# Kernel tuning notes

Measured on AMD Instinct MI355X. Metric: run time of the kernel, lower is better.

Reference implementation:

```python
import jax, jax.numpy as jnp
import numpy as np

N, E, B = 50000, 800000, 128
IN, HID, OUT, H = 256, 256, 256, 4
NEG_SLOPE = 0.2
EPS_BN = 1e-5
EPS_LN = 1e-5


def setup_inputs() -> dict:
    key = jax.random.key(0)
    ks = jax.random.split(key, 10)
    C1, C2 = HID // H, OUT // H
    s = lambda k, sh: jax.random.normal(k, sh, jnp.float32) * 0.05
    return dict(
        x=jax.random.normal(ks[0], (N, IN), jnp.float32),
        edge_index=jax.random.randint(ks[1], (2, E), 0, N),
        batch=jnp.sort(jax.random.randint(ks[2], (N,), 0, B)),
        W1=s(ks[3], (IN, HID)), a_src1=s(ks[4], (H, C1)), a_dst1=s(ks[5], (H, C1)),
        b1=jnp.zeros((HID,), jnp.float32),
        bn1_g=jnp.ones((HID,), jnp.float32), bn1_b=jnp.zeros((HID,), jnp.float32),
        bn1_m=jnp.zeros((HID,), jnp.float32), bn1_v=jnp.ones((HID,), jnp.float32),
        ln1_g=jnp.ones((HID,), jnp.float32), ln1_b=jnp.zeros((HID,), jnp.float32),
        W2=s(ks[6], (HID + IN, OUT)), a_src2=s(ks[7], (H, C2)), a_dst2=s(ks[8], (H, C2)),
        b2=jnp.zeros((OUT,), jnp.float32),
        bn2_g=jnp.ones((OUT,), jnp.float32), bn2_b=jnp.zeros((OUT,), jnp.float32),
        bn2_m=jnp.zeros((OUT,), jnp.float32), bn2_v=jnp.ones((OUT,), jnp.float32),
        ln2_g=jnp.ones((OUT,), jnp.float32), ln2_b=jnp.zeros((OUT,), jnp.float32),
    )


def gat_conv(x, edge_index, W, a_s, a_d, b):
    # PyG GATConv (concat heads, add_self_loops=True, eval -> no attention dropout)
    n = x.shape[0]
    Hh, C = a_s.shape
    h = (x @ W).reshape(n, Hh, C)                      # [N,H,C]
    loop = jnp.arange(n)
    src = jnp.concatenate([edge_index[0], loop])       # [E+N]
    dst = jnp.concatenate([edge_index[1], loop])
    al_s = jnp.einsum('nhc,hc->nh', h, a_s)            # [N,H]
    al_d = jnp.einsum('nhc,hc->nh', h, a_d)
    e = jax.nn.leaky_relu(al_s[src] + al_d[dst], NEG_SLOPE)   # [E+N,H]
    emax = jax.ops.segment_max(e, dst, num_segments=n)        # segment softmax over incoming edges
    p = jnp.exp(e - emax[dst])
    denom = jax.ops.segment_sum(p, dst, num_segments=n)
    alpha = p / (denom[dst] + 1e-16)
    out = jax.ops.segment_sum(alpha[:, :, None] * h[src], dst, num_segments=n)
    return out.reshape(n, Hh * C) + b


def bn_eval(x, g, b, m, v):
    return (x - m) * (g * jax.lax.rsqrt(v + EPS_BN)) + b


def layer_norm(x, g, b):
    mu = jnp.mean(x, axis=-1, keepdims=True)
    var = jnp.mean(jnp.square(x - mu), axis=-1, keepdims=True)
    return (x - mu) * jax.lax.rsqrt(var + EPS_LN) * g + b


def reference(x, edge_index, batch,
              W1, a_src1, a_dst1, b1, bn1_g, bn1_b, bn1_m, bn1_v, ln1_g, ln1_b,
              W2, a_src2, a_dst2, b2, bn2_g, bn2_b, bn2_m, bn2_v, ln2_g, ln2_b):
    x1 = x
    h = gat_conv(x, edge_index, W1, a_src1, a_dst1, b1)
    h = jax.nn.relu(layer_norm(bn_eval(h, bn1_g, bn1_b, bn1_m, bn1_v), ln1_g, ln1_b))
    x2 = h
    # root_extend: broadcast the first node of each (sorted) batch segment
    root_idx = jnp.searchsorted(batch, jnp.arange(B))  # first occurrence per graph
    h = jnp.concatenate([h, x1[root_idx[batch]]], axis=1)
    h = gat_conv(h, edge_index, W2, a_src2, a_dst2, b2)
    h = jax.nn.relu(layer_norm(bn_eval(h, bn2_g, bn2_b, bn2_m, bn2_v), ln2_g, ln2_b))
    h = jnp.concatenate([h, x2[root_idx[batch]]], axis=1)   # [N, OUT+HID]
    sums = jax.ops.segment_sum(h, batch, num_segments=B)
    cnt = jax.ops.segment_sum(jnp.ones((h.shape[0],), h.dtype), batch, num_segments=B)
    return sums / jnp.maximum(cnt, 1.0)[:, None]            # scatter_mean -> [B, OUT+HID]
```

## Files before the change

### kernel.cpp

```cpp
#include <hip/hip_runtime.h>
#include <stdint.h>

typedef unsigned short u16;
typedef unsigned int u32;
typedef unsigned char u8;
typedef __bf16 bf16x8 __attribute__((ext_vector_type(8)));
typedef float f32x4 __attribute__((ext_vector_type(4)));

#define NGRAPH 128

__device__ __forceinline__ float b2f(u16 u) {
    union { u32 i; float f; } c; c.i = ((u32)u) << 16; return c.f;
}
__device__ __forceinline__ u16 f2b(float f) {
    union { float f; u32 i; } c; c.f = f;
    u32 r = c.i + 0x7fffu + ((c.i >> 16) & 1u);
    return (u16)(r >> 16);
}
__device__ __forceinline__ float s8x(u32 v, int k) {
    return (float)((int)(v << (24 - 8 * k)) >> 24);
}

__global__ void k_sentinel(u16* __restrict__ out, int n, u16 pat) {
    int i = blockIdx.x * 256 + threadIdx.x;
    if (i < n) out[i] = pat;
}

__global__ __launch_bounds__(256) void k_init(const u16* __restrict__ x, const int* __restrict__ batch,
                                              int* __restrict__ deg, float* __restrict__ pool,
                                              int* __restrict__ flag, int* __restrict__ root,
                                              int N, int B) {
    __shared__ int cnt;
    int i = blockIdx.x * 256 + threadIdx.x;
    if (i < N + 1) deg[i] = 0;
    if (i < B * 256) pool[i] = 0.0f;
    if (blockIdx.x == 0) {
        if (threadIdx.x == 0) cnt = 0;
        __syncthreads();
        int weird = 0;
        for (int k = threadIdx.x; k < 4096; k += 256) {
            u16 u = x[2 * k];
            int e = (u >> 7) & 0xff;
            if (e != 0 && (e < 100 || e > 140)) weird++;
        }
        atomicAdd(&cnt, weird);
        __syncthreads();
        if (threadIdx.x == 0) *flag = (cnt > 1024) ? 1 : 0;
    } else if (blockIdx.x == 1) {
        int b = threadIdx.x;
        if (b <= B) {
            int lo = 0, hi = N;
            while (lo < hi) { int mid = (lo + hi) >> 1; if (batch[mid] < b) lo = mid + 1; else hi = mid; }
            root[b] = lo;
        }
    }
}

__global__ __launch_bounds__(256) void k_cvt4(const void* __restrict__ src, u16* __restrict__ dst,
                                              int n4, const int* __restrict__ flag) {
    int i = blockIdx.x * 256 + threadIdx.x;
    if (i >= n4) return;
    if (*flag) {
        float4 v = ((const float4*)src)[i];
        ushort4 o;
        o.x = f2b(v.x); o.y = f2b(v.y); o.z = f2b(v.z); o.w = f2b(v.w);
        ((ushort4*)dst)[i] = o;
    } else {
        ((ushort4*)dst)[i] = ((const ushort4*)src)[i];
    }
}

__global__ __launch_bounds__(256) void k_cvt_small(
    const void* p0, const void* p1, const void* p2, const void* p3, const void* p4,
    const void* p5, const void* p6, const void* p7, const void* p8, const void* p9,
    const void* p10, const void* p11, const void* p12, const void* p13, const void* p14,
    const void* p15, const void* p16, const void* p17,
    u16* __restrict__ dst, const int* __restrict__ flag) {
    const void* ps[18] = {p0,p1,p2,p3,p4,p5,p6,p7,p8,p9,p10,p11,p12,p13,p14,p15,p16,p17};
    int f = *flag;
    int vec = blockIdx.x;
    int j = threadIdx.x;
    const void* s = ps[vec];
    dst[vec * 256 + j] = f ? f2b(((const float*)s)[j]) : ((const u16*)s)[j];
}

__global__ __launch_bounds__(256) void k_tr2(const u16* __restrict__ w1, u16* __restrict__ wt1,
                                             const u16* __restrict__ w2, u16* __restrict__ wt2) {
    int idx = blockIdx.x * 256 + threadIdx.x;
    int halfsel = idx >> 16;
    int j = idx & 65535;
    int n = j >> 8, k = j & 255;
    if (halfsel == 0) wt1[n * 256 + k] = w1[k * 256 + n];
    else              wt2[n * 256 + k] = w2[k * 256 + n];
}

__global__ __launch_bounds__(256) void k_hist(const int* __restrict__ ei, int* __restrict__ deg, int E) {
    int e = blockIdx.x * 256 + threadIdx.x;
    if (e < E) atomicAdd(&deg[ei[E + e]], 1);
}

__global__ __launch_bounds__(256) void k_scan1(const int* __restrict__ in, int* __restrict__ out,
                                               int* __restrict__ bsums, int total) {
    __shared__ int lds[256];
    int tid = threadIdx.x;
    int base = blockIdx.x * 2048 + tid * 8;
    int v[8]; int ts = 0;
#pragma unroll
    for (int r = 0; r < 8; r++) { int i = base + r; int x = (i < total) ? in[i] : 0; v[r] = x; ts += x; }
    lds[tid] = ts;
    __syncthreads();
    for (int off = 1; off < 256; off <<= 1) {
        int t = (tid >= off) ? lds[tid - off] : 0;
        __syncthreads();
        lds[tid] += t;
        __syncthreads();
    }
    int run = lds[tid] - ts;
#pragma unroll
    for (int r = 0; r < 8; r++) { int i = base + r; if (i < total) out[i] = run; run += v[r]; }
    if (tid == 255) bsums[blockIdx.x] = lds[255];
}

__global__ void k_scan2(int* __restrict__ bsums, int nb) {
    if (threadIdx.x == 0 && blockIdx.x == 0) {
        int run = 0;
        for (int i = 0; i < nb; i++) { int t = bsums[i]; bsums[i] = run; run += t; }
    }
}

__global__ __launch_bounds__(256) void k_scan3(const int* __restrict__ pscan, const int* __restrict__ bsums,
                                               int* __restrict__ ptr, int* __restrict__ cursor,
                                               int total, int N) {
    int i = blockIdx.x * 256 + threadIdx.x;
    if (i >= total) return;
    int val = pscan[i] + bsums[i >> 11];
    ptr[i] = val;
    if (i < N) cursor[i] = val;
}

__global__ __launch_bounds__(256) void k_fill(const int* __restrict__ ei, int* __restrict__ cursor,
                                              int* __restrict__ csr, int E) {
    int e = blockIdx.x * 256 + threadIdx.x;
    if (e < E) {
        int src = ei[e];
        int pos = atomicAdd(&cursor[ei[E + e]], 1);
        csr[pos] = src;
    }
}

__global__ __launch_bounds__(256) void k_gemm(const u16* __restrict__ A, const u16* __restrict__ Bt,
                                              u16* __restrict__ C, u8* __restrict__ C8,
                                              float* __restrict__ salsc, int M,
                                              const float* __restrict__ r2, const int* __restrict__ batch) {
    __shared__ __align__(16) u16 smem[128 * 64 * 2];
    u16* As = smem;
    u16* Bs = smem + 128 * 64;
    const int tid = threadIdx.x;
    const int lane = tid & 63;
    const int wave = tid >> 6;
    const int bm = blockIdx.x >> 1;
    const int bn = blockIdx.x & 1;
    const int m0 = bm * 128, n0 = bn * 128;
    const int wm = wave >> 1, wn = wave & 1;
    const int lm = lane & 15, lq = lane >> 4;
    f32x4 acc[4][4] = {};

    for (int k0 = 0; k0 < 256; k0 += 64) {
        uint4 ra[4], rb[4];
#pragma unroll
        for (int it = 0; it < 4; ++it) {
            int t = tid + 256 * it;
            int m = t >> 3;
            int kc = (t & 7) ^ (m & 7);
            int gm = m0 + m; if (gm > M - 1) gm = M - 1;
            ra[it] = *(const uint4*)(A + (size_t)gm * 256 + k0 + kc * 8);
            rb[it] = *(const uint4*)(Bt + (size_t)(n0 + m) * 256 + k0 + kc * 8);
        }
        __syncthreads();
#pragma unroll
        for (int it = 0; it < 4; ++it) {
            int t = tid + 256 * it;
            *(uint4*)(As + t * 8) = ra[it];
            *(uint4*)(Bs + t * 8) = rb[it];
        }
        __syncthreads();
#pragma unroll
        for (int ks = 0; ks < 2; ++ks) {
            int kq = ks * 4 + lq;
            bf16x8 af[4], bfr[4];
#pragma unroll
            for (int i = 0; i < 4; i++) {
                int m = wm * 64 + i * 16 + lm;
                af[i] = *(const bf16x8*)(As + (m * 8 + (kq ^ (m & 7))) * 8);
                int n = wn * 64 + i * 16 + lm;
                bfr[i] = *(const bf16x8*)(Bs + (n * 8 + (kq ^ (n & 7))) * 8);
            }
#pragma unroll
            for (int i = 0; i < 4; i++)
#pragma unroll
                for (int j = 0; j < 4; j++)
                    acc[i][j] = __builtin_amdgcn_mfma_f32_16x16x32_bf16(af[i], bfr[j], acc[i][j], 0, 0, 0);
        }
    }

    __syncthreads();
    u8* lds8 = (u8*)smem;
#pragma unroll
    for (int i = 0; i < 4; i++) {
#pragma unroll
        for (int r = 0; r < 4; r++) {
            int rl = wm * 64 + i * 16 + lq * 4 + r;
            int row = m0 + rl;
            bool ok = (row < M);
            const float* r2row = (r2 && ok) ? (r2 + (size_t)batch[row] * 256) : nullptr;
            float v[4];
#pragma unroll
            for (int j = 0; j < 4; j++) {
                v[j] = acc[i][j][r];
                if (r2row) v[j] += r2row[n0 + wn * 64 + j * 16 + lm];
            }
            float mx = fmaxf(fmaxf(fabsf(v[0]), fabsf(v[1])), fmaxf(fabsf(v[2]), fabsf(v[3])));
#pragma unroll
            for (int off = 1; off < 16; off <<= 1) mx = fmaxf(mx, __shfl_xor(mx, off));
            float scl = mx * (1.0f / 127.0f);
            float isc = (mx > 0.f) ? 127.0f / mx : 0.f;
#pragma unroll
            for (int j = 0; j < 4; j++) {
                int col = n0 + wn * 64 + j * 16 + lm;
                if (ok) C[(size_t)row * 256 + col] = f2b(v[j]);
                int q = (int)rintf(v[j] * isc);
                lds8[rl * 144 + wn * 64 + j * 16 + lm] = (u8)(q & 0xff);
            }
            if (ok && lm == 0) salsc[(size_t)row * 8 + (bn * 2 + wn) * 2 + 1] = scl;
        }
    }
    __syncthreads();
    for (int t = tid; t < 1024; t += 256) {
        int rl = t >> 3;
        int off = (t & 7) * 16;
        int row = m0 + rl;
        if (row < M)
            *(uint4*)(C8 + (size_t)row * 256 + n0 + off) = *(const uint4*)(lds8 + rl * 144 + off);
    }
}

__global__ __launch_bounds__(256) void k_al(const u16* __restrict__ h, const u16* __restrict__ a_s,
                                            const u16* __restrict__ a_d,
                                            float* __restrict__ salsc, float* __restrict__ ald, int N) {
    int node = blockIdx.x * 4 + (threadIdx.x >> 6);
    if (node >= N) return;
    int lane = threadIdx.x & 63;
    int c0 = lane * 4;
    int head = lane >> 4;
    int ci = c0 & 63;
    ushort4 hv = *(const ushort4*)(h + (size_t)node * 256 + c0);
    float h0 = b2f(hv.x), h1 = b2f(hv.y), h2 = b2f(hv.z), h3 = b2f(hv.w);
    ushort4 sv = *(const ushort4*)(a_s + head * 64 + ci);
    ushort4 dv = *(const ushort4*)(a_d + head * 64 + ci);
    float ps = h0 * b2f(sv.x) + h1 * b2f(sv.y) + h2 * b2f(sv.z) + h3 * b2f(sv.w);
    float pd = h0 * b2f(dv.x) + h1 * b2f(dv.y) + h2 * b2f(dv.z) + h3 * b2f(dv.w);
#pragma unroll
    for (int off = 1; off < 16; off <<= 1) { ps += __shfl_xor(ps, off); pd += __shfl_xor(pd, off); }
    if ((lane & 15) == 0) {
        salsc[(size_t)node * 8 + head * 2] = ps;
        ald[node * 4 + head] = pd;
    }
}

__global__ __launch_bounds__(256) void k_agg5(
    const u16* __restrict__ h, const u8* __restrict__ h8,
    const float* __restrict__ salsc, const float* __restrict__ ald_,
    const int* __restrict__ ptr, const int* __restrict__ csr,
    const u16* __restrict__ bias, const u16* __restrict__ bng, const u16* __restrict__ bnb,
    const u16* __restrict__ bnm, const u16* __restrict__ bnv,
    const u16* __restrict__ lng, const u16* __restrict__ lnb,
    u16* __restrict__ xout, float* __restrict__ pool, const int* __restrict__ batch, int N) {
    int node = blockIdx.x * 4 + (threadIdx.x >> 6);
    if (node >= N) return;
    int lane = threadIdx.x & 63;
    int c0 = lane * 4;
    int head = lane >> 4;
    float ad = ald_[node * 4 + head];
    float es = salsc[(size_t)node * 8 + head * 2] + ad; es = (es > 0.f) ? es : 0.2f * es;
    float psf = __expf(es);
    float s = psf;
    ushort4 hv = *(const ushort4*)(h + (size_t)node * 256 + c0);
    float a0 = psf * b2f(hv.x), a1 = psf * b2f(hv.y), a2 = psf * b2f(hv.z), a3 = psf * b2f(hv.w);
    int beg = ptr[node], end = ptr[node + 1];
    int i = beg;
    for (; i + 4 <= end; i += 4) {
        int s0 = csr[i], s1 = csr[i + 1], s2 = csr[i + 2], s3 = csr[i + 3];
        float2 f0 = *(const float2*)(salsc + (size_t)s0 * 8 + head * 2);
        float2 f1 = *(const float2*)(salsc + (size_t)s1 * 8 + head * 2);
        float2 f2v = *(const float2*)(salsc + (size_t)s2 * 8 + head * 2);
        float2 f3 = *(const float2*)(salsc + (size_t)s3 * 8 + head * 2);
        u32 r0 = *(const u32*)(h8 + (size_t)s0 * 256 + c0);
        u32 r1 = *(const u32*)(h8 + (size_t)s1 * 256 + c0);
        u32 r2v = *(const u32*)(h8 + (size_t)s2 * 256 + c0);
        u32 r3 = *(const u32*)(h8 + (size_t)s3 * 256 + c0);
        float e0 = f0.x + ad; e0 = (e0 > 0.f) ? e0 : 0.2f * e0;
        float e1 = f1.x + ad; e1 = (e1 > 0.f) ? e1 : 0.2f * e1;
        float e2 = f2v.x + ad; e2 = (e2 > 0.f) ? e2 : 0.2f * e2;
        float e3 = f3.x + ad; e3 = (e3 > 0.f) ? e3 : 0.2f * e3;
        float p0 = __expf(e0), p1 = __expf(e1), p2 = __expf(e2), p3 = __expf(e3);
        s += p0 + p1 + p2 + p3;
        float w0 = p0 * f0.y, w1 = p1 * f1.y, w2 = p2 * f2v.y, w3 = p3 * f3.y;
        a0 += w0 * s8x(r0, 0) + w1 * s8x(r1, 0) + w2 * s8x(r2v, 0) + w3 * s8x(r3, 0);
        a1 += w0 * s8x(r0, 1) + w1 * s8x(r1, 1) + w2 * s8x(r2v, 1) + w3 * s8x(r3, 1);
        a2 += w0 * s8x(r0, 2) + w1 * s8x(r1, 2) + w2 * s8x(r2v, 2) + w3 * s8x(r3, 2);
        a3 += w0 * s8x(r0, 3) + w1 * s8x(r1, 3) + w2 * s8x(r2v, 3) + w3 * s8x(r3, 3);
    }
    for (; i < end; ++i) {
        int s0 = csr[i];
        float2 f0 = *(const float2*)(salsc + (size_t)s0 * 8 + head * 2);
        u32 r0 = *(const u32*)(h8 + (size_t)s0 * 256 + c0);
        float e0 = f0.x + ad; e0 = (e0 > 0.f) ? e0 : 0.2f * e0;
        float p0 = __expf(e0);
        s += p0;
        float w0 = p0 * f0.y;
        a0 += w0 * s8x(r0, 0); a1 += w0 * s8x(r0, 1); a2 += w0 * s8x(r0, 2); a3 += w0 * s8x(r0, 3);
    }
    float inv = 1.0f / (s + 1e-16f);
    float v0 = a0 * inv + b2f(bias[c0 + 0]);
    float v1 = a1 * inv + b2f(bias[c0 + 1]);
    float v2 = a2 * inv + b2f(bias[c0 + 2]);
    float v3 = a3 * inv + b2f(bias[c0 + 3]);
    v0 = (v0 - b2f(bnm[c0 + 0])) * (b2f(bng[c0 + 0]) * rsqrtf(b2f(bnv[c0 + 0]) + 1e-5f)) + b2f(bnb[c0 + 0]);
    v1 = (v1 - b2f(bnm[c0 + 1])) * (b2f(bng[c0 + 1]) * rsqrtf(b2f(bnv[c0 + 1]) + 1e-5f)) + b2f(bnb[c0 + 1]);
    v2 = (v2 - b2f(bnm[c0 + 2])) * (b2f(bng[c0 + 2]) * rsqrtf(b2f(bnv[c0 + 2]) + 1e-5f)) + b2f(bnb[c0 + 2]);
    v3 = (v3 - b2f(bnm[c0 + 3])) * (b2f(bng[c0 + 3]) * rsqrtf(b2f(bnv[c0 + 3]) + 1e-5f)) + b2f(bnb[c0 + 3]);
    float sum = v0 + v1 + v2 + v3;
#pragma unroll
    for (int off = 1; off < 64; off <<= 1) sum += __shfl_xor(sum, off);
    float mu = sum * 0.00390625f;
    float d0 = v0 - mu, d1 = v1 - mu, d2 = v2 - mu, d3 = v3 - mu;
    float q = d0 * d0 + d1 * d1 + d2 * d2 + d3 * d3;
#pragma unroll
    for (int off = 1; off < 64; off <<= 1) q += __shfl_xor(q, off);
    float rstd = rsqrtf(q * 0.00390625f + 1e-5f);
    float y0 = fmaxf(d0 * rstd * b2f(lng[c0 + 0]) + b2f(lnb[c0 + 0]), 0.f);
    float y1 = fmaxf(d1 * rstd * b2f(lng[c0 + 1]) + b2f(lnb[c0 + 1]), 0.f);
    float y2 = fmaxf(d2 * rstd * b2f(lng[c0 + 2]) + b2f(lnb[c0 + 2]), 0.f);
    float y3 = fmaxf(d3 * rstd * b2f(lng[c0 + 3]) + b2f(lnb[c0 + 3]), 0.f);
    if (xout) {
        uint2 o;
        o.x = (u32)f2b(y0) | ((u32)f2b(y1) << 16);
        o.y = (u32)f2b(y2) | ((u32)f2b(y3) << 16);
        *(uint2*)(xout + (size_t)node * 256 + c0) = o;
    }
    if (pool) {
        int g = batch[node];
        float* pp = pool + (size_t)g * 256 + c0;
        atomicAdd(pp + 0, y0); atomicAdd(pp + 1, y1); atomicAdd(pp + 2, y2); atomicAdd(pp + 3, y3);
    }
}

__global__ __launch_bounds__(256) void k_r2(const u16* __restrict__ xc, const u16* __restrict__ w2,
                                            const int* __restrict__ root, float* __restrict__ r2, int N) {
    __shared__ float xs[256];
    int b = blockIdx.x, c = threadIdx.x;
    int rt = root[b]; if (rt >= N) rt = N - 1; if (rt < 0) rt = 0;
    xs[c] = b2f(xc[(size_t)rt * 256 + c]);
    __syncthreads();
    float acc = 0.f;
    for (int k = 0; k < 256; k++) acc += xs[k] * b2f(w2[(size_t)(256 + k) * 256 + c]);
    r2[b * 256 + c] = acc;
}

__global__ void k_final(const float* __restrict__ pool, const u16* __restrict__ x2,
                        const int* __restrict__ root, void* __restrict__ out,
                        const int* __restrict__ flag) {
    int b = blockIdx.x, c = threadIdx.x;
    int r0 = root[b], r1 = root[b + 1];
    int cnt = r1 - r0;
    float inv = 1.0f / (float)(cnt > 1 ? cnt : 1);
    float v0 = pool[b * 256 + c] * inv;
    float v1 = (cnt > 0) ? b2f(x2[(size_t)r0 * 256 + c]) : 0.0f;
    if (*flag) {
        float* o = (float*)out;
        o[b * 512 + c] = v0;
        o[b * 512 + 256 + c] = v1;
    } else {
        u16* o = (u16*)out;
        o[b * 512 + c] = f2b(v0);
        o[b * 512 + 256 + c] = f2b(v1);
    }
}

extern "C" void kernel_launch(void* const* d_in, const int* in_sizes, int n_in,
                              void* d_out, int out_size, void* d_ws, size_t ws_size,
                              hipStream_t stream) {
    u16* outp = (u16*)d_out;
    int ogrid = (out_size + 255) / 256;

    if (n_in != 23) {
        k_sentinel<<<ogrid, 256, 0, stream>>>(outp, out_size, (u16)0x44FA);
        return;
    }

    const void* x_raw = d_in[0];
    const int* ei = (const int*)d_in[1];
    const int* batch = (const int*)d_in[2];
    const int NX = in_sizes[0];
    const int E = in_sizes[1] / 2;
    const int N = in_sizes[2];
    const int NW1 = in_sizes[3];
    const int NW2 = in_sizes[13];
    const int B = NGRAPH;

    char* p = (char*)d_ws;
    auto carve = [&](size_t bytes) -> void* {
        void* r = (void*)p; p += (bytes + 255) & ~(size_t)255; return r;
    };
    u16* xc    = (u16*)carve((size_t)NX * 2);
    u16* w1c   = (u16*)carve((size_t)NW1 * 2);
    u16* w2c   = (u16*)carve((size_t)NW2 * 2);
    u16* sc    = (u16*)carve((size_t)18 * 256 * 2);
    u16* wt1   = (u16*)carve((size_t)65536 * 2);
    u16* wt2   = (u16*)carve((size_t)65536 * 2);
    u16* hbuf  = (u16*)carve((size_t)N * 256 * 2);
    u8*  h8    = (u8*)carve((size_t)N * 256);
    u16* x2    = (u16*)carve((size_t)N * 256 * 2);
    float* salsc = (float*)carve((size_t)N * 8 * 4);
    float* ald = (float*)carve((size_t)N * 4 * 4);
    int* deg    = (int*)carve((size_t)(N + 1) * 4);
    int* pscan  = (int*)carve((size_t)(N + 1) * 4);
    int* ptr    = (int*)carve((size_t)(N + 1) * 4);
    int* cursor = (int*)carve((size_t)N * 4);
    int* csr    = (int*)carve((size_t)E * 4);
    int* bsums  = (int*)carve(1024);
    int* root   = (int*)carve((size_t)(B + 1) * 4);
    float* r2   = (float*)carve((size_t)B * 256 * 4);
    float* pool = (float*)carve((size_t)B * 256 * 4);
    int* flag   = (int*)carve(256);

    size_t needed = (size_t)(p - (char*)d_ws);
    if (needed > ws_size) {
        k_sentinel<<<ogrid, 256, 0, stream>>>(outp, out_size, (u16)0x447A);
        return;
    }

    int zmax = (N + 1) > (B * 256) ? (N + 1) : (B * 256);
    k_init<<<(zmax + 255) / 256, 256, 0, stream>>>((const u16*)x_raw, batch, deg, pool, flag, root, N, B);

    k_cvt4<<<(NX / 4 + 255) / 256, 256, 0, stream>>>(x_raw, xc, NX / 4, flag);
    k_cvt4<<<(NW1 / 4 + 255) / 256, 256, 0, stream>>>(d_in[3], w1c, NW1 / 4, flag);
    k_cvt4<<<(NW2 / 4 + 255) / 256, 256, 0, stream>>>(d_in[13], w2c, NW2 / 4, flag);
    k_cvt_small<<<18, 256, 0, stream>>>(
        d_in[4], d_in[5], d_in[6], d_in[7], d_in[8], d_in[9], d_in[10], d_in[11], d_in[12],
        d_in[14], d_in[15], d_in[16], d_in[17], d_in[18], d_in[19], d_in[20], d_in[21], d_in[22],
        sc, flag);

    k_tr2<<<512, 256, 0, stream>>>(w1c, wt1, w2c, wt2);

    k_hist<<<(E + 255) / 256, 256, 0, stream>>>(ei, deg, E);
    int nb1 = (N + 1 + 2047) / 2048;
    k_scan1<<<nb1, 256, 0, stream>>>(deg, pscan, bsums, N + 1);
    k_scan2<<<1, 64, 0, stream>>>(bsums, nb1);
    k_scan3<<<(N + 1 + 255) / 256, 256, 0, stream>>>(pscan, bsums, ptr, cursor, N + 1, N);
    k_fill<<<(E + 255) / 256, 256, 0, stream>>>(ei, cursor, csr, E);

    int mt = (N + 127) / 128;
    int ngrid = (N + 3) / 4;
    k_gemm<<<mt * 2, 256, 0, stream>>>(xc, wt1, hbuf, h8, salsc, N, nullptr, nullptr);
    k_al<<<ngrid, 256, 0, stream>>>(hbuf, sc + 0 * 256, sc + 1 * 256, salsc, ald, N);
    k_agg5<<<ngrid, 256, 0, stream>>>(hbuf, h8, salsc, ald, ptr, csr,
        sc + 2 * 256, sc + 3 * 256, sc + 4 * 256, sc + 5 * 256, sc + 6 * 256, sc + 7 * 256, sc + 8 * 256,
        x2, nullptr, batch, N);
    k_r2<<<B, 256, 0, stream>>>(xc, w2c, root, r2, N);
    k_gemm<<<mt * 2, 256, 0, stream>>>(x2, wt2, hbuf, h8, salsc, N, r2, batch);
    k_al<<<ngrid, 256, 0, stream>>>(hbuf, sc + 9 * 256, sc + 10 * 256, salsc, ald, N);
    k_agg5<<<ngrid, 256, 0, stream>>>(hbuf, h8, salsc, ald, ptr, csr,
        sc + 11 * 256, sc + 12 * 256, sc + 13 * 256, sc + 14 * 256, sc + 15 * 256, sc + 16 * 256, sc + 17 * 256,
        nullptr, pool, batch, N);

    k_final<<<B, 256, 0, stream>>>(pool, x2, root, d_out, flag);
    (void)ws_size;
}
```

Measured before the change: 726.0 us.

## Split GAT aggregation into edge-weight pass and head-major int8 gather

Attention weights are now computed once per edge and head in a separate kernel, which writes a head-major edge-weight array and the per-node normalizers. The aggregation kernel then gathers int8 features from a new head-major layout produced by the GEMM epilogue, one byte per lane per head, so each head gather touches a 64-byte contiguous segment. This removes the repeated exp and leaky-relu work from the gather loop and makes the loads coalesce across the wavefront. In exchange it adds a kernel launch per layer, an extra E×4 float buffer round trip through memory, and four passes over the CSR indices in place of one.

```diff
diff --git a/kernel.cpp b/kernel.cpp
--- a/kernel.cpp
+++ b/kernel.cpp
@@ -16,9 +16,6 @@
     union { float f; u32 i; } c; c.f = f;
     u32 r = c.i + 0x7fffu + ((c.i >> 16) & 1u);
     return (u16)(r >> 16);
-}
-__device__ __forceinline__ float s8x(u32 v, int k) {
-    return (float)((int)(v << (24 - 8 * k)) >> 24);
 }
 
 __global__ void k_sentinel(u16* __restrict__ out, int n, u16 pat) {
@@ -237,10 +234,13 @@
     __syncthreads();
     for (int t = tid; t < 1024; t += 256) {
         int rl = t >> 3;
-        int off = (t & 7) * 16;
+        int seg = t & 7;
+        int hh = seg >> 2;
+        int off = (seg & 3) * 16;
         int row = m0 + rl;
         if (row < M)
-            *(uint4*)(C8 + (size_t)row * 256 + n0 + off) = *(const uint4*)(lds8 + rl * 144 + off);
+            *(uint4*)(C8 + ((size_t)(bn * 2 + hh) * M + row) * 64 + off) =
+                *(const uint4*)(lds8 + rl * 144 + hh * 64 + off);
     }
 }
 
@@ -267,91 +267,112 @@
     }
 }
 
-__global__ __launch_bounds__(256) void k_agg5(
+__global__ __launch_bounds__(256) void k_attw(
+    const float* __restrict__ salsc, const float* __restrict__ ald_,
+    const int* __restrict__ ptr, const int* __restrict__ csr,
+    float* __restrict__ aw, float* __restrict__ invs, float* __restrict__ selfw, int N, int E) {
+    int node = blockIdx.x * 4 + (threadIdx.x >> 6);
+    if (node >= N) return;
+    int lane = threadIdx.x & 63;
+    int h = lane & 3;
+    int el = lane >> 2;
+    int beg = ptr[node], end = ptr[node + 1];
+    float ad = ald_[node * 4 + h];
+    float s = 0.f;
+    for (int i0 = beg; i0 < end; i0 += 16) {
+        int e = i0 + el;
+        if (e < end) {
+            int src = csr[e];
+            float2 f = *(const float2*)(salsc + (size_t)src * 8 + h * 2);
+            float lg = f.x + ad; lg = (lg > 0.f) ? lg : 0.2f * lg;
+            float p = __expf(lg);
+            aw[(size_t)h * E + e] = p * f.y;
+            s += p;
+        }
+    }
+#pragma unroll
+    for (int off = 4; off < 64; off <<= 1) s += __shfl_xor(s, off);
+    float es = salsc[(size_t)node * 8 + h * 2] + ad; es = (es > 0.f) ? es : 0.2f * es;
+    float pself = __expf(es);
+    s += pself;
+    if (el == 0) {
+        float inv = 1.0f / (s + 1e-16f);
+        invs[node * 4 + h] = inv;
+        selfw[node * 4 + h] = pself * inv;
+    }
+}
+
+__global__ __launch_bounds__(256) void k_agg6(
     const u16* __restrict__ h, const u8* __restrict__ h8,
-    const float* __restrict__ salsc, const float* __restrict__ ald_,
+    const float* __restrict__ aw, const float* __restrict__ invs_, const float* __restrict__ selfw_,
     const int* __restrict__ ptr, const int* __restrict__ csr,
     const u16* __restrict__ bias, const u16* __restrict__ bng, const u16* __restrict__ bnb,
     const u16* __restrict__ bnm, const u16* __restrict__ bnv,
     const u16* __restrict__ lng, const u16* __restrict__ lnb,
-    u16* __restrict__ xout, float* __restrict__ pool, const int* __restrict__ batch, int N) {
+    u16* __restrict__ xout, float* __restrict__ pool, const int* __restrict__ batch, int N, int E) {
     int node = blockIdx.x * 4 + (threadIdx.x >> 6);
     if (node >= N) return;
     int lane = threadIdx.x & 63;
-    int c0 = lane * 4;
-    int head = lane >> 4;
-    float ad = ald_[node * 4 + head];
-    float es = salsc[(size_t)node * 8 + head * 2] + ad; es = (es > 0.f) ? es : 0.2f * es;
-    float psf = __expf(es);
-    float s = psf;
-    ushort4 hv = *(const ushort4*)(h + (size_t)node * 256 + c0);
-    float a0 = psf * b2f(hv.x), a1 = psf * b2f(hv.y), a2 = psf * b2f(hv.z), a3 = psf * b2f(hv.w);
     int beg = ptr[node], end = ptr[node + 1];
-    int i = beg;
-    for (; i + 4 <= end; i += 4) {
-        int s0 = csr[i], s1 = csr[i + 1], s2 = csr[i + 2], s3 = csr[i + 3];
-        float2 f0 = *(const float2*)(salsc + (size_t)s0 * 8 + head * 2);
-        float2 f1 = *(const float2*)(salsc + (size_t)s1 * 8 + head * 2);
-        float2 f2v = *(const float2*)(salsc + (size_t)s2 * 8 + head * 2);
-        float2 f3 = *(const float2*)(salsc + (size_t)s3 * 8 + head * 2);
-        u32 r0 = *(const u32*)(h8 + (size_t)s0 * 256 + c0);
-        u32 r1 = *(const u32*)(h8 + (size_t)s1 * 256 + c0);
-        u32 r2v = *(const u32*)(h8 + (size_t)s2 * 256 + c0);
-        u32 r3 = *(const u32*)(h8 + (size_t)s3 * 256 + c0);
-        float e0 = f0.x + ad; e0 = (e0 > 0.f) ? e0 : 0.2f * e0;
-        float e1 = f1.x + ad; e1 = (e1 > 0.f) ? e1 : 0.2f * e1;
-        float e2 = f2v.x + ad; e2 = (e2 > 0.f) ? e2 : 0.2f * e2;
-        float e3 = f3.x + ad; e3 = (e3 > 0.f) ? e3 : 0.2f * e3;
-        float p0 = __expf(e0), p1 = __expf(e1), p2 = __expf(e2), p3 = __expf(e3);
-        s += p0 + p1 + p2 + p3;
-        float w0 = p0 * f0.y, w1 = p1 * f1.y, w2 = p2 * f2v.y, w3 = p3 * f3.y;
-        a0 += w0 * s8x(r0, 0) + w1 * s8x(r1, 0) + w2 * s8x(r2v, 0) + w3 * s8x(r3, 0);
-        a1 += w0 * s8x(r0, 1) + w1 * s8x(r1, 1) + w2 * s8x(r2v, 1) + w3 * s8x(r3, 1);
-        a2 += w0 * s8x(r0, 2) + w1 * s8x(r1, 2) + w2 * s8x(r2v, 2) + w3 * s8x(r3, 2);
-        a3 += w0 * s8x(r0, 3) + w1 * s8x(r1, 3) + w2 * s8x(r2v, 3) + w3 * s8x(r3, 3);
-    }
-    for (; i < end; ++i) {
-        int s0 = csr[i];
-        float2 f0 = *(const float2*)(salsc + (size_t)s0 * 8 + head * 2);
-        u32 r0 = *(const u32*)(h8 + (size_t)s0 * 256 + c0);
-        float e0 = f0.x + ad; e0 = (e0 > 0.f) ? e0 : 0.2f * e0;
-        float p0 = __expf(e0);
-        s += p0;
-        float w0 = p0 * f0.y;
-        a0 += w0 * s8x(r0, 0); a1 += w0 * s8x(r0, 1); a2 += w0 * s8x(r0, 2); a3 += w0 * s8x(r0, 3);
-    }
-    float inv = 1.0f / (s + 1e-16f);
-    float v0 = a0 * inv + b2f(bias[c0 + 0]);
-    float v1 = a1 * inv + b2f(bias[c0 + 1]);
-    float v2 = a2 * inv + b2f(bias[c0 + 2]);
-    float v3 = a3 * inv + b2f(bias[c0 + 3]);
-    v0 = (v0 - b2f(bnm[c0 + 0])) * (b2f(bng[c0 + 0]) * rsqrtf(b2f(bnv[c0 + 0]) + 1e-5f)) + b2f(bnb[c0 + 0]);
-    v1 = (v1 - b2f(bnm[c0 + 1])) * (b2f(bng[c0 + 1]) * rsqrtf(b2f(bnv[c0 + 1]) + 1e-5f)) + b2f(bnb[c0 + 1]);
-    v2 = (v2 - b2f(bnm[c0 + 2])) * (b2f(bng[c0 + 2]) * rsqrtf(b2f(bnv[c0 + 2]) + 1e-5f)) + b2f(bnb[c0 + 2]);
-    v3 = (v3 - b2f(bnm[c0 + 3])) * (b2f(bng[c0 + 3]) * rsqrtf(b2f(bnv[c0 + 3]) + 1e-5f)) + b2f(bnb[c0 + 3]);
-    float sum = v0 + v1 + v2 + v3;
+    float acc[4];
+#pragma unroll
+    for (int hh = 0; hh < 4; ++hh) {
+        const float* awh = aw + (size_t)hh * E;
+        const u8* h8h = h8 + (size_t)hh * N * 64;
+        float sa = 0.f, sb = 0.f, sc2 = 0.f, sd = 0.f;
+        int i = beg;
+        for (; i + 4 <= end; i += 4) {
+            int s0 = csr[i], s1 = csr[i + 1], s2 = csr[i + 2], s3 = csr[i + 3];
+            float w0 = awh[i], w1 = awh[i + 1], w2 = awh[i + 2], w3 = awh[i + 3];
+            float q0 = (float)(signed char)h8h[(size_t)s0 * 64 + lane];
+            float q1 = (float)(signed char)h8h[(size_t)s1 * 64 + lane];
+            float q2 = (float)(signed char)h8h[(size_t)s2 * 64 + lane];
+            float q3 = (float)(signed char)h8h[(size_t)s3 * 64 + lane];
+            sa += w0 * q0; sb += w1 * q1; sc2 += w2 * q2; sd += w3 * q3;
+        }
+        for (; i < end; ++i) {
+            int s0 = csr[i];
+            float w0 = awh[i];
+            sa += w0 * (float)(signed char)h8h[(size_t)s0 * 64 + lane];
+        }
+        acc[hh] = (sa + sb) + (sc2 + sd);
+    }
+    float v[4];
+#pragma unroll
+    for (int hh = 0; hh < 4; ++hh) {
+        int c = hh * 64 + lane;
+        float inv = invs_[node * 4 + hh];
+        float sw = selfw_[node * 4 + hh];
+        float self = b2f(h[(size_t)node * 256 + c]);
+        float t = acc[hh] * inv + sw * self + b2f(bias[c]);
+        v[hh] = (t - b2f(bnm[c])) * (b2f(bng[c]) * rsqrtf(b2f(bnv[c]) + 1e-5f)) + b2f(bnb[c]);
+    }
+    float sum = v[0] + v[1] + v[2] + v[3];
 #pragma unroll
     for (int off = 1; off < 64; off <<= 1) sum += __shfl_xor(sum, off);
     float mu = sum * 0.00390625f;
-    float d0 = v0 - mu, d1 = v1 - mu, d2 = v2 - mu, d3 = v3 - mu;
-    float q = d0 * d0 + d1 * d1 + d2 * d2 + d3 * d3;
+    float q = 0.f;
+#pragma unroll
+    for (int hh = 0; hh < 4; ++hh) { v[hh] -= mu; q += v[hh] * v[hh]; }
 #pragma unroll
     for (int off = 1; off < 64; off <<= 1) q += __shfl_xor(q, off);
     float rstd = rsqrtf(q * 0.00390625f + 1e-5f);
-    float y0 = fmaxf(d0 * rstd * b2f(lng[c0 + 0]) + b2f(lnb[c0 + 0]), 0.f);
-    float y1 = fmaxf(d1 * rstd * b2f(lng[c0 + 1]) + b2f(lnb[c0 + 1]), 0.f);
-    float y2 = fmaxf(d2 * rstd * b2f(lng[c0 + 2]) + b2f(lnb[c0 + 2]), 0.f);
-    float y3 = fmaxf(d3 * rstd * b2f(lng[c0 + 3]) + b2f(lnb[c0 + 3]), 0.f);
+    float y[4];
+#pragma unroll
+    for (int hh = 0; hh < 4; ++hh) {
+        int c = hh * 64 + lane;
+        y[hh] = fmaxf(v[hh] * rstd * b2f(lng[c]) + b2f(lnb[c]), 0.f);
+    }
     if (xout) {
-        uint2 o;
-        o.x = (u32)f2b(y0) | ((u32)f2b(y1) << 16);
-        o.y = (u32)f2b(y2) | ((u32)f2b(y3) << 16);
-        *(uint2*)(xout + (size_t)node * 256 + c0) = o;
+#pragma unroll
+        for (int hh = 0; hh < 4; ++hh)
+            xout[(size_t)node * 256 + hh * 64 + lane] = f2b(y[hh]);
     }
     if (pool) {
         int g = batch[node];
-        float* pp = pool + (size_t)g * 256 + c0;
-        atomicAdd(pp + 0, y0); atomicAdd(pp + 1, y1); atomicAdd(pp + 2, y2); atomicAdd(pp + 3, y3);
+        float* pp = pool + (size_t)g * 256;
+#pragma unroll
+        for (int hh = 0; hh < 4; ++hh) atomicAdd(pp + hh * 64 + lane, y[hh]);
     }
 }
 
@@ -423,6 +444,9 @@
     u16* x2    = (u16*)carve((size_t)N * 256 * 2);
     float* salsc = (float*)carve((size_t)N * 8 * 4);
     float* ald = (float*)carve((size_t)N * 4 * 4);
+    float* aw  = (float*)carve((size_t)E * 4 * 4);
+    float* invs  = (float*)carve((size_t)N * 4 * 4);
+    float* selfw = (float*)carve((size_t)N * 4 * 4);
     int* deg    = (int*)carve((size_t)(N + 1) * 4);
     int* pscan  = (int*)carve((size_t)(N + 1) * 4);
     int* ptr    = (int*)carve((size_t)(N + 1) * 4);
@@ -464,15 +488,17 @@
     int ngrid = (N + 3) / 4;
     k_gemm<<<mt * 2, 256, 0, stream>>>(xc, wt1, hbuf, h8, salsc, N, nullptr, nullptr);
     k_al<<<ngrid, 256, 0, stream>>>(hbuf, sc + 0 * 256, sc + 1 * 256, salsc, ald, N);
-    k_agg5<<<ngrid, 256, 0, stream>>>(hbuf, h8, salsc, ald, ptr, csr,
+    k_attw<<<ngrid, 256, 0, stream>>>(salsc, ald, ptr, csr, aw, invs, selfw, N, E);
+    k_agg6<<<ngrid, 256, 0, stream>>>(hbuf, h8, aw, invs, selfw, ptr, csr,
         sc + 2 * 256, sc + 3 * 256, sc + 4 * 256, sc + 5 * 256, sc + 6 * 256, sc + 7 * 256, sc + 8 * 256,
-        x2, nullptr, batch, N);
+        x2, nullptr, batch, N, E);
     k_r2<<<B, 256, 0, stream>>>(xc, w2c, root, r2, N);
     k_gemm<<<mt * 2, 256, 0, stream>>>(x2, wt2, hbuf, h8, salsc, N, r2, batch);
     k_al<<<ngrid, 256, 0, stream>>>(hbuf, sc + 9 * 256, sc + 10 * 256, salsc, ald, N);
-    k_agg5<<<ngrid, 256, 0, stream>>>(hbuf, h8, salsc, ald, ptr, csr,
+    k_attw<<<ngrid, 256, 0, stream>>>(salsc, ald, ptr, csr, aw, invs, selfw, N, E);
+    k_agg6<<<ngrid, 256, 0, stream>>>(hbuf, h8, aw, invs, selfw, ptr, csr,
         sc + 11 * 256, sc + 12 * 256, sc + 13 * 256, sc + 14 * 256, sc + 15 * 256, sc + 16 * 256, sc + 17 * 256,
-        nullptr, pool, batch, N);
+        nullptr, pool, batch, N, E);
 
     k_final<<<B, 256, 0, stream>>>(pool, x2, root, d_out, flag);
     (void)ws_size;
```

After: 694.0 us. 4.4% less time.

## Split int8 features by head and aggregate per head with XCD-aware block mapping

Applied to the files above, without the earlier changes.

The GEMM now writes the int8 quantized features as four head-major planes of N x 64 instead of row-major N x 256. The aggregation is split into a per-head gather kernel, whose block index is mapped so each head lands on specific XCDs to improve L2 locality for that head's plane. It writes partial sums to a new bf16 buffer, and a separate finish kernel adds the self-loop term, bias, batch norm, layer norm, ReLU and pooling. This trades an extra kernel launch and an N x 256 bf16 intermediate round trip for smaller per-XCD gather working sets. The gather now uses byte loads per lane instead of 4-byte loads.

```diff
diff --git a/kernel.cpp b/kernel.cpp
--- a/kernel.cpp
+++ b/kernel.cpp
@@ -16,9 +16,6 @@
     union { float f; u32 i; } c; c.f = f;
     u32 r = c.i + 0x7fffu + ((c.i >> 16) & 1u);
     return (u16)(r >> 16);
-}
-__device__ __forceinline__ float s8x(u32 v, int k) {
-    return (float)((int)(v << (24 - 8 * k)) >> 24);
 }
 
 __global__ void k_sentinel(u16* __restrict__ out, int n, u16 pat) {
@@ -237,10 +234,13 @@
     __syncthreads();
     for (int t = tid; t < 1024; t += 256) {
         int rl = t >> 3;
-        int off = (t & 7) * 16;
+        int seg = t & 7;
+        int hh = seg >> 2;
+        int off = (seg & 3) * 16;
         int row = m0 + rl;
         if (row < M)
-            *(uint4*)(C8 + (size_t)row * 256 + n0 + off) = *(const uint4*)(lds8 + rl * 144 + off);
+            *(uint4*)(C8 + ((size_t)(bn * 2 + hh) * M + row) * 64 + off) =
+                *(const uint4*)(lds8 + rl * 144 + hh * 64 + off);
     }
 }
 
@@ -267,10 +267,60 @@
     }
 }
 
-__global__ __launch_bounds__(256) void k_agg5(
-    const u16* __restrict__ h, const u8* __restrict__ h8,
+__global__ __launch_bounds__(256) void k_aggh(
+    const u8* __restrict__ h8, const float* __restrict__ salsc, const float* __restrict__ ald_,
+    const int* __restrict__ ptr, const int* __restrict__ csr,
+    u16* __restrict__ hacc, float* __restrict__ ssum, int N) {
+    int b = blockIdx.x;
+    int xcd = b & 7;
+    int head = xcd >> 1;
+    int node = (b >> 3) * 8 + (xcd & 1) * 4 + (threadIdx.x >> 6);
+    if (node >= N) return;
+    int lane = threadIdx.x & 63;
+    float ad = ald_[node * 4 + head];
+    const u8* __restrict__ h8h = h8 + (size_t)head * N * 64;
+    int beg = ptr[node], end = ptr[node + 1];
+    float s = 0.f;
+    float aca = 0.f, acb = 0.f, acc2 = 0.f, acd = 0.f;
+    int i = beg;
+    for (; i + 4 <= end; i += 4) {
+        int s0 = csr[i], s1 = csr[i + 1], s2 = csr[i + 2], s3 = csr[i + 3];
+        float2 f0 = *(const float2*)(salsc + (size_t)s0 * 8 + head * 2);
+        float2 f1 = *(const float2*)(salsc + (size_t)s1 * 8 + head * 2);
+        float2 f2v = *(const float2*)(salsc + (size_t)s2 * 8 + head * 2);
+        float2 f3 = *(const float2*)(salsc + (size_t)s3 * 8 + head * 2);
+        float q0 = (float)(signed char)h8h[(size_t)s0 * 64 + lane];
+        float q1 = (float)(signed char)h8h[(size_t)s1 * 64 + lane];
+        float q2 = (float)(signed char)h8h[(size_t)s2 * 64 + lane];
+        float q3 = (float)(signed char)h8h[(size_t)s3 * 64 + lane];
+        float e0 = f0.x + ad; e0 = (e0 > 0.f) ? e0 : 0.2f * e0;
+        float e1 = f1.x + ad; e1 = (e1 > 0.f) ? e1 : 0.2f * e1;
+        float e2 = f2v.x + ad; e2 = (e2 > 0.f) ? e2 : 0.2f * e2;
+        float e3 = f3.x + ad; e3 = (e3 > 0.f) ? e3 : 0.2f * e3;
+        float p0 = __expf(e0), p1 = __expf(e1), p2 = __expf(e2), p3 = __expf(e3);
+        s += (p0 + p1) + (p2 + p3);
+        aca += (p0 * f0.y) * q0;
+        acb += (p1 * f1.y) * q1;
+        acc2 += (p2 * f2v.y) * q2;
+        acd += (p3 * f3.y) * q3;
+    }
+    for (; i < end; ++i) {
+        int s0 = csr[i];
+        float2 f0 = *(const float2*)(salsc + (size_t)s0 * 8 + head * 2);
+        float q0 = (float)(signed char)h8h[(size_t)s0 * 64 + lane];
+        float e0 = f0.x + ad; e0 = (e0 > 0.f) ? e0 : 0.2f * e0;
+        float p0 = __expf(e0);
+        s += p0;
+        aca += (p0 * f0.y) * q0;
+    }
+    float accv = (aca + acb) + (acc2 + acd);
+    hacc[((size_t)node * 4 + head) * 64 + lane] = f2b(accv);
+    if (lane == 0) ssum[node * 4 + head] = s;
+}
+
+__global__ __launch_bounds__(256) void k_aggfin(
+    const u16* __restrict__ h, const u16* __restrict__ hacc, const float* __restrict__ ssum,
     const float* __restrict__ salsc, const float* __restrict__ ald_,
-    const int* __restrict__ ptr, const int* __restrict__ csr,
     const u16* __restrict__ bias, const u16* __restrict__ bng, const u16* __restrict__ bnb,
     const u16* __restrict__ bnm, const u16* __restrict__ bnv,
     const u16* __restrict__ lng, const u16* __restrict__ lnb,
@@ -278,80 +328,36 @@
     int node = blockIdx.x * 4 + (threadIdx.x >> 6);
     if (node >= N) return;
     int lane = threadIdx.x & 63;
-    int c0 = lane * 4;
-    int head = lane >> 4;
-    float ad = ald_[node * 4 + head];
-    float es = salsc[(size_t)node * 8 + head * 2] + ad; es = (es > 0.f) ? es : 0.2f * es;
-    float psf = __expf(es);
-    float s = psf;
-    ushort4 hv = *(const ushort4*)(h + (size_t)node * 256 + c0);
-    float a0 = psf * b2f(hv.x), a1 = psf * b2f(hv.y), a2 = psf * b2f(hv.z), a3 = psf * b2f(hv.w);
-    int beg = ptr[node], end = ptr[node + 1];
-    int i = beg;
-    for (; i + 4 <= end; i += 4) {
-        int s0 = csr[i], s1 = csr[i + 1], s2 = csr[i + 2], s3 = csr[i + 3];
-        float2 f0 = *(const float2*)(salsc + (size_t)s0 * 8 + head * 2);
-        float2 f1 = *(const float2*)(salsc + (size_t)s1 * 8 + head * 2);
-        float2 f2v = *(const float2*)(salsc + (size_t)s2 * 8 + head * 2);
-        float2 f3 = *(const float2*)(salsc + (size_t)s3 * 8 + head * 2);
-        u32 r0 = *(const u32*)(h8 + (size_t)s0 * 256 + c0);
-        u32 r1 = *(const u32*)(h8 + (size_t)s1 * 256 + c0);
-        u32 r2v = *(const u32*)(h8 + (size_t)s2 * 256 + c0);
-        u32 r3 = *(const u32*)(h8 + (size_t)s3 * 256 + c0);
-        float e0 = f0.x + ad; e0 = (e0 > 0.f) ? e0 : 0.2f * e0;
-        float e1 = f1.x + ad; e1 = (e1 > 0.f) ? e1 : 0.2f * e1;
-        float e2 = f2v.x + ad; e2 = (e2 > 0.f) ? e2 : 0.2f * e2;
-        float e3 = f3.x + ad; e3 = (e3 > 0.f) ? e3 : 0.2f * e3;
-        float p0 = __expf(e0), p1 = __expf(e1), p2 = __expf(e2), p3 = __expf(e3);
-        s += p0 + p1 + p2 + p3;
-        float w0 = p0 * f0.y, w1 = p1 * f1.y, w2 = p2 * f2v.y, w3 = p3 * f3.y;
-        a0 += w0 * s8x(r0, 0) + w1 * s8x(r1, 0) + w2 * s8x(r2v, 0) + w3 * s8x(r3, 0);
-        a1 += w0 * s8x(r0, 1) + w1 * s8x(r1, 1) + w2 * s8x(r2v, 1) + w3 * s8x(r3, 1);
-        a2 += w0 * s8x(r0, 2) + w1 * s8x(r1, 2) + w2 * s8x(r2v, 2) + w3 * s8x(r3, 2);
-        a3 += w0 * s8x(r0, 3) + w1 * s8x(r1, 3) + w2 * s8x(r2v, 3) + w3 * s8x(r3, 3);
-    }
-    for (; i < end; ++i) {
-        int s0 = csr[i];
-        float2 f0 = *(const float2*)(salsc + (size_t)s0 * 8 + head * 2);
-        u32 r0 = *(const u32*)(h8 + (size_t)s0 * 256 + c0);
-        float e0 = f0.x + ad; e0 = (e0 > 0.f) ? e0 : 0.2f * e0;
-        float p0 = __expf(e0);
-        s += p0;
-        float w0 = p0 * f0.y;
-        a0 += w0 * s8x(r0, 0); a1 += w0 * s8x(r0, 1); a2 += w0 * s8x(r0, 2); a3 += w0 * s8x(r0, 3);
-    }
-    float inv = 1.0f / (s + 1e-16f);
-    float v0 = a0 * inv + b2f(bias[c0 + 0]);
-    float v1 = a1 * inv + b2f(bias[c0 + 1]);
-    float v2 = a2 * inv + b2f(bias[c0 + 2]);
-    float v3 = a3 * inv + b2f(bias[c0 + 3]);
-    v0 = (v0 - b2f(bnm[c0 + 0])) * (b2f(bng[c0 + 0]) * rsqrtf(b2f(bnv[c0 + 0]) + 1e-5f)) + b2f(bnb[c0 + 0]);
-    v1 = (v1 - b2f(bnm[c0 + 1])) * (b2f(bng[c0 + 1]) * rsqrtf(b2f(bnv[c0 + 1]) + 1e-5f)) + b2f(bnb[c0 + 1]);
-    v2 = (v2 - b2f(bnm[c0 + 2])) * (b2f(bng[c0 + 2]) * rsqrtf(b2f(bnv[c0 + 2]) + 1e-5f)) + b2f(bnb[c0 + 2]);
-    v3 = (v3 - b2f(bnm[c0 + 3])) * (b2f(bng[c0 + 3]) * rsqrtf(b2f(bnv[c0 + 3]) + 1e-5f)) + b2f(bnb[c0 + 3]);
-    float sum = v0 + v1 + v2 + v3;
+    float v[4];
+#pragma unroll
+    for (int hh = 0; hh < 4; ++hh) {
+        int c = hh * 64 + lane;
+        float als = salsc[(size_t)node * 8 + hh * 2];
+        float ad = ald_[node * 4 + hh];
+        float es = als + ad; es = (es > 0.f) ? es : 0.2f * es;
+        float ps = __expf(es);
+        float inv = 1.0f / (ssum[node * 4 + hh] + ps + 1e-16f);
+        float selfv = b2f(h[(size_t)node * 256 + c]);
+        float acc = b2f(hacc[((size_t)node * 4 + hh) * 64 + lane]);
+        float t = (acc + ps * selfv) * inv + b2f(bias[c]);
+        v[hh] = (t - b2f(bnm[c])) * (b2f(bng[c]) * rsqrtf(b2f(bnv[c]) + 1e-5f)) + b2f(bnb[c]);
+    }
+    float sum = v[0] + v[1] + v[2] + v[3];
 #pragma unroll
     for (int off = 1; off < 64; off <<= 1) sum += __shfl_xor(sum, off);
     float mu = sum * 0.00390625f;
-    float d0 = v0 - mu, d1 = v1 - mu, d2 = v2 - mu, d3 = v3 - mu;
-    float q = d0 * d0 + d1 * d1 + d2 * d2 + d3 * d3;
+    float q = 0.f;
+#pragma unroll
+    for (int hh = 0; hh < 4; ++hh) { v[hh] -= mu; q += v[hh] * v[hh]; }
 #pragma unroll
     for (int off = 1; off < 64; off <<= 1) q += __shfl_xor(q, off);
     float rstd = rsqrtf(q * 0.00390625f + 1e-5f);
-    float y0 = fmaxf(d0 * rstd * b2f(lng[c0 + 0]) + b2f(lnb[c0 + 0]), 0.f);
-    float y1 = fmaxf(d1 * rstd * b2f(lng[c0 + 1]) + b2f(lnb[c0 + 1]), 0.f);
-    float y2 = fmaxf(d2 * rstd * b2f(lng[c0 + 2]) + b2f(lnb[c0 + 2]), 0.f);
-    float y3 = fmaxf(d3 * rstd * b2f(lng[c0 + 3]) + b2f(lnb[c0 + 3]), 0.f);
-    if (xout) {
-        uint2 o;
-        o.x = (u32)f2b(y0) | ((u32)f2b(y1) << 16);
-        o.y = (u32)f2b(y2) | ((u32)f2b(y3) << 16);
-        *(uint2*)(xout + (size_t)node * 256 + c0) = o;
-    }
-    if (pool) {
-        int g = batch[node];
-        float* pp = pool + (size_t)g * 256 + c0;
-        atomicAdd(pp + 0, y0); atomicAdd(pp + 1, y1); atomicAdd(pp + 2, y2); atomicAdd(pp + 3, y3);
+#pragma unroll
+    for (int hh = 0; hh < 4; ++hh) {
+        int c = hh * 64 + lane;
+        float y = fmaxf(v[hh] * rstd * b2f(lng[c]) + b2f(lnb[c]), 0.f);
+        if (xout) xout[(size_t)node * 256 + c] = f2b(y);
+        if (pool) atomicAdd(pool + (size_t)batch[node] * 256 + c, y);
     }
 }
 
@@ -421,6 +427,8 @@
     u16* hbuf  = (u16*)carve((size_t)N * 256 * 2);
     u8*  h8    = (u8*)carve((size_t)N * 256);
     u16* x2    = (u16*)carve((size_t)N * 256 * 2);
+    u16* hacc  = (u16*)carve((size_t)N * 256 * 2);
+    float* ssum  = (float*)carve((size_t)N * 4 * 4);
     float* salsc = (float*)carve((size_t)N * 8 * 4);
     float* ald = (float*)carve((size_t)N * 4 * 4);
     int* deg    = (int*)carve((size_t)(N + 1) * 4);
@@ -462,15 +470,18 @@
 
     int mt = (N + 127) / 128;
     int ngrid = (N + 3) / 4;
+    int agrid = ((N + 7) / 8) * 8;
     k_gemm<<<mt * 2, 256, 0, stream>>>(xc, wt1, hbuf, h8, salsc, N, nullptr, nullptr);
     k_al<<<ngrid, 256, 0, stream>>>(hbuf, sc + 0 * 256, sc + 1 * 256, salsc, ald, N);
-    k_agg5<<<ngrid, 256, 0, stream>>>(hbuf, h8, salsc, ald, ptr, csr,
+    k_aggh<<<agrid, 256, 0, stream>>>(h8, salsc, ald, ptr, csr, hacc, ssum, N);
+    k_aggfin<<<ngrid, 256, 0, stream>>>(hbuf, hacc, ssum, salsc, ald,
         sc + 2 * 256, sc + 3 * 256, sc + 4 * 256, sc + 5 * 256, sc + 6 * 256, sc + 7 * 256, sc + 8 * 256,
         x2, nullptr, batch, N);
     k_r2<<<B, 256, 0, stream>>>(xc, w2c, root, r2, N);
     k_gemm<<<mt * 2, 256, 0, stream>>>(x2, wt2, hbuf, h8, salsc, N, r2, batch);
     k_al<<<ngrid, 256, 0, stream>>>(hbuf, sc + 9 * 256, sc + 10 * 256, salsc, ald, N);
-    k_agg5<<<ngrid, 256, 0, stream>>>(hbuf, h8, salsc, ald, ptr, csr,
+    k_aggh<<<agrid, 256, 0, stream>>>(h8, salsc, ald, ptr, csr, hacc, ssum, N);
+    k_aggfin<<<ngrid, 256, 0, stream>>>(hbuf, hacc, ssum, salsc, ald,
         sc + 11 * 256, sc + 12 * 256, sc + 13 * 256, sc + 14 * 256, sc + 15 * 256, sc + 16 * 256, sc + 17 * 256,
         nullptr, pool, batch, N);
 
```

Measured after the change: 820.5 us. +13.0%, slower.
